# Performance work log

Hardware: AMD Instinct MI355X
Metric: run time of the kernel (lower is better)

The kernel has to match this reference:

```python
import jax, jax.numpy as jnp
import numpy as np

DIM = 4096
N_HEADS = 32
HEAD_DIM = 128
N_KV = 8
REP = N_HEADS // N_KV  # 4
B = 8       # number of packed sequences (block-diagonal blocks)
S = 1024    # tokens per sequence
T = B * S   # seqlen_sum = 8192


def setup_inputs() -> dict:
    key = jax.random.key(0)
    ks = jax.random.split(key, 6)
    x = jax.random.normal(ks[0], (T, DIM), dtype=jnp.float32)
    # RoPE freqs: positions restart at 0 for each packed sequence
    pos = jnp.tile(jnp.arange(S, dtype=jnp.float32), B)            # [T]
    inv_freq = 1.0 / (10000.0 ** (jnp.arange(0, HEAD_DIM, 2, dtype=jnp.float32) / HEAD_DIM))  # [HEAD_DIM//2]
    freqs = pos[:, None] * inv_freq[None, :]                       # [T, HEAD_DIM//2]
    cos = jnp.cos(freqs)
    sin = jnp.sin(freqs)
    s = 0.02
    wq = jax.random.normal(ks[1], (DIM, N_HEADS * HEAD_DIM), dtype=jnp.float32) * s
    wk = jax.random.normal(ks[2], (DIM, N_KV * HEAD_DIM), dtype=jnp.float32) * s
    wv = jax.random.normal(ks[3], (DIM, N_KV * HEAD_DIM), dtype=jnp.float32) * s
    wo = jax.random.normal(ks[4], (N_HEADS * HEAD_DIM, DIM), dtype=jnp.float32) * s
    return {"x": x, "cos": cos, "sin": sin, "wq": wq, "wk": wk, "wv": wv, "wo": wo}


def _rope(t, cos, sin):
    # t: [T, H, D]; cos/sin: [T, D//2]; complex rotation on (even, odd) pairs
    th, hd = t.shape[1], t.shape[2]
    tp = t.reshape(t.shape[0], th, hd // 2, 2)
    te, to = tp[..., 0], tp[..., 1]
    c = cos[:, None, :]
    s = sin[:, None, :]
    oe = te * c - to * s
    oo = te * s + to * c
    return jnp.stack([oe, oo], axis=-1).reshape(t.shape)


def reference(x, cos, sin, wq, wk, wv, wo):
    scale = HEAD_DIM ** -0.5
    q = (x @ wq).reshape(T, N_HEADS, HEAD_DIM)
    k = (x @ wk).reshape(T, N_KV, HEAD_DIM)
    v = (x @ wv).reshape(T, N_KV, HEAD_DIM)
    q = _rope(q, cos, sin)
    k = _rope(k, cos, sin)
    # Block-diagonal mask with equal blocks == batched attention over B sequences.
    # GQA: q head index h = kv*REP + r (matches repeat_interleave on kv dim),
    # so group q heads as [N_KV, REP] instead of materializing repeated K/V.
    q = q.reshape(B, S, N_KV, REP, HEAD_DIM)
    k = k.reshape(B, S, N_KV, HEAD_DIM)
    v = v.reshape(B, S, N_KV, HEAD_DIM)
    scores = jnp.einsum('bqkrd,bskd->bkrqs', q, k) * scale   # [B, N_KV, REP, S, S]
    attn = jax.nn.softmax(scores, axis=-1)
    out = jnp.einsum('bkrqs,bskd->bqkrd', attn, v)           # [B, S, N_KV, REP, D]
    out = out.reshape(T, N_HEADS * HEAD_DIM)
    return out @ wo
```

## Files before the change

### kernel.cpp

```cpp
#include <hip/hip_runtime.h>
#include <math.h>

typedef unsigned short ushort_t;
typedef __attribute__((ext_vector_type(8))) short short8;
typedef __attribute__((ext_vector_type(4))) float f32x4;

#define MFMA16(a, b, c) __builtin_amdgcn_mfma_f32_16x16x32_bf16(a, b, c, 0, 0, 0)

__device__ __forceinline__ ushort_t f2bf(float f) {
    union { float f; unsigned u; } v;
    v.f = f;
    unsigned r = v.u + 0x7FFF + ((v.u >> 16) & 1);
    return (ushort_t)(r >> 16);
}

__device__ __forceinline__ void gload_lds16(const ushort_t* g, ushort_t* l) {
    __builtin_amdgcn_global_load_lds(
        (const __attribute__((address_space(1))) void*)g,
        (__attribute__((address_space(3))) void*)l, 16, 0, 0);
}

__global__ __launch_bounds__(256) void cast_f32_bf16(const float* __restrict__ src,
                                                     ushort_t* __restrict__ dst, int n8) {
    int i = blockIdx.x * 256 + threadIdx.x;
    if (i >= n8) return;
    const float4* s = (const float4*)src;
    float4 a = s[2 * i], b = s[2 * i + 1];
    union { ushort_t u[8]; uint4 v; } o;
    o.u[0] = f2bf(a.x); o.u[1] = f2bf(a.y); o.u[2] = f2bf(a.z); o.u[3] = f2bf(a.w);
    o.u[4] = f2bf(b.x); o.u[5] = f2bf(b.y); o.u[6] = f2bf(b.z); o.u[7] = f2bf(b.w);
    ((uint4*)dst)[i] = o.v;
}

__global__ __launch_bounds__(256) void transpose_cast(const float* __restrict__ src,
                                                      int D, int N,
                                                      ushort_t* __restrict__ dst, int dstStride) {
    __shared__ float t[32][33];
    int n0 = blockIdx.x * 32, d0 = blockIdx.y * 32;
    int tx = threadIdx.x & 31, ty = threadIdx.x >> 5;
#pragma unroll
    for (int i = 0; i < 4; i++)
        t[ty + 8 * i][tx] = src[(size_t)(d0 + ty + 8 * i) * N + n0 + tx];
    __syncthreads();
#pragma unroll
    for (int i = 0; i < 4; i++) {
        int n = ty + 8 * i;
        dst[(size_t)(n0 + n) * dstStride + d0 + tx] = f2bf(t[tx][n]);
    }
}

__global__ __launch_bounds__(256) void transpose_v(const ushort_t* __restrict__ qkv,
                                                   ushort_t* __restrict__ vt) {
    __shared__ ushort_t t[32][33];
    int bk = blockIdx.z; int b = bk >> 3, kvh = bk & 7;
    int s0 = blockIdx.x * 32, d0 = blockIdx.y * 32;
    int tx = threadIdx.x & 31, ty = threadIdx.x >> 5;
#pragma unroll
    for (int i = 0; i < 4; i++)
        t[ty + 8 * i][tx] = qkv[(size_t)(b * 1024 + s0 + ty + 8 * i) * 6144 + 5120 + kvh * 128 + d0 + tx];
    __syncthreads();
#pragma unroll
    for (int i = 0; i < 4; i++)
        vt[((size_t)(b * 8 + kvh) * 128 + d0 + ty + 8 * i) * 1024 + s0 + tx] = t[tx][ty + 8 * i];
}

template <int EPI>
__global__ __launch_bounds__(512, 2) void gemm8x(
    const ushort_t* __restrict__ A, const ushort_t* __restrict__ Bt,
    ushort_t* __restrict__ obf, float* __restrict__ of32,
    int M, int N, int K,
    const float* __restrict__ cosT, const float* __restrict__ sinT) {
    extern __shared__ __align__(16) ushort_t lds[];
    const int tid = threadIdx.x;
    const int lane = tid & 63, wv = tid >> 6;
    const int wr = wv >> 2, wc = wv & 3;
    const int lr = lane & 15, g = lane >> 4;

    const int gx = gridDim.x;
    const int nwg = gx * gridDim.y;
    const int bid = blockIdx.y * gx + blockIdx.x;
    const int swz = (bid & 7) * (nwg >> 3) + (bid >> 3);
    const int brow = (swz / gx) * 256, bcol = (swz % gx) * 256;

    const int st_r = tid >> 3, st_p = tid & 7;
    const int cA = (st_p ^ (st_r & 7)) * 8;
    const size_t aS0 = (size_t)(brow + st_r) * K + cA;
    const size_t bS0 = (size_t)(bcol + st_r) * K + cA;
    const int dstT = st_r * 64 + st_p * 8;

    const int sl0 = (g ^ (lr & 7)) * 8;
    const int sl1 = ((4 + g) ^ (lr & 7)) * 8;
    const int aRow = (wr * 128 + lr) * 64;
    const int bRow = (wc * 64 + lr) * 64;

    f32x4 acc[8][4];
#pragma unroll
    for (int m = 0; m < 8; m++)
#pragma unroll
        for (int n = 0; n < 4; n++) acc[m][n] = (f32x4){0.f, 0.f, 0.f, 0.f};

#define STG_A(kn, roff)                                                          \
    gload_lds16(A + aS0 + (size_t)(roff) * K + (size_t)(kn) * 64,                \
                lds + ((kn) & 1) * 16384 + (roff) * 64 + dstT)
#define STG_B(kn, roff)                                                          \
    gload_lds16(Bt + bS0 + (size_t)(roff) * K + (size_t)(kn) * 64,               \
                lds + 32768 + ((kn) & 1) * 16384 + (roff) * 64 + dstT)

    STG_B(0, 0);  STG_B(0, 64);
    STG_B(0, 128); STG_B(0, 192);
    STG_A(0, 0);  STG_A(0, 128);
    STG_A(0, 64); STG_A(0, 192);

    const int NKT = K >> 6;
    for (int kt = 0; kt < NKT; ++kt) {
        const int buf = (kt & 1) * 16384;
        const bool stg = kt < NKT - 1;
        const int kn = kt + 1;

        asm volatile("s_waitcnt vmcnt(2)" ::: "memory");
        __builtin_amdgcn_sched_barrier(0);
        __builtin_amdgcn_s_barrier();
        __builtin_amdgcn_sched_barrier(0);
        if (stg) { STG_B(kn, 0); STG_B(kn, 64); STG_B(kn, 128); STG_B(kn, 192); }
        short8 bfr[2][4], af[2][4];
#pragma unroll
        for (int n = 0; n < 4; ++n) {
            bfr[0][n] = *(const short8*)(lds + 32768 + buf + bRow + n * 1024 + sl0);
            bfr[1][n] = *(const short8*)(lds + 32768 + buf + bRow + n * 1024 + sl1);
        }
#pragma unroll
        for (int m = 0; m < 4; ++m) {
            af[0][m] = *(const short8*)(lds + buf + aRow + m * 1024 + sl0);
            af[1][m] = *(const short8*)(lds + buf + aRow + m * 1024 + sl1);
        }
        __builtin_amdgcn_s_setprio(1);
#pragma unroll
        for (int ks = 0; ks < 2; ++ks)
#pragma unroll
            for (int m = 0; m < 4; ++m)
#pragma unroll
                for (int n = 0; n < 4; ++n)
                    acc[m][n] = MFMA16(af[ks][m], bfr[ks][n], acc[m][n]);
        __builtin_amdgcn_s_setprio(0);

        if (stg) asm volatile("s_waitcnt vmcnt(4)" ::: "memory");
        else     asm volatile("s_waitcnt vmcnt(0)" ::: "memory");
        __builtin_amdgcn_sched_barrier(0);
        __builtin_amdgcn_s_barrier();
        __builtin_amdgcn_sched_barrier(0);
        if (stg) { STG_A(kn, 0); STG_A(kn, 128); STG_A(kn, 64); STG_A(kn, 192); }
#pragma unroll
        for (int m = 0; m < 4; ++m) {
            af[0][m] = *(const short8*)(lds + buf + aRow + 4096 + m * 1024 + sl0);
            af[1][m] = *(const short8*)(lds + buf + aRow + 4096 + m * 1024 + sl1);
        }
        __builtin_amdgcn_s_setprio(1);
#pragma unroll
        for (int ks = 0; ks < 2; ++ks)
#pragma unroll
            for (int m = 0; m < 4; ++m)
#pragma unroll
                for (int n = 0; n < 4; ++n)
                    acc[m + 4][n] = MFMA16(af[ks][m], bfr[ks][n], acc[m + 4][n]);
        __builtin_amdgcn_s_setprio(0);
    }
#undef STG_A
#undef STG_B

#pragma unroll
    for (int m = 0; m < 8; ++m) {
#pragma unroll
        for (int n = 0; n < 4; ++n) {
#pragma unroll
            for (int reg = 0; reg < 4; ++reg) {
                int r = brow + wr * 128 + m * 16 + g * 4 + reg;
                int c = bcol + wc * 64 + n * 16 + lr;
                float val = acc[m][n][reg];
                if (EPI == 1) {
                    float other = __shfl_xor(val, 1, 64);
                    if (c < 5120) {
                        int pos = r & 1023;
                        int pair = (c & 127) >> 1;
                        float cz = cosT[pos * 64 + pair];
                        float sz = sinT[pos * 64 + pair];
                        val = val * cz + other * ((c & 1) ? sz : -sz);
                        if (c < 4096) val *= 0.12752551286084110f;
                    }
                    obf[(size_t)r * N + c] = f2bf(val);
                } else {
                    of32[(size_t)r * N + c] = val;
                }
            }
        }
    }
}

__global__ __launch_bounds__(512, 2) void attn_fwd2(const ushort_t* __restrict__ qkv,
                                                    const ushort_t* __restrict__ vt,
                                                    ushort_t* __restrict__ aout) {
    extern __shared__ __align__(16) ushort_t lds[];
    const int tid = threadIdx.x, lane = tid & 63, w = tid >> 6;
    const int lr = lane & 15, g = lane >> 4;
    const int hr = w & 3, qc = w >> 2;
    const int qt = blockIdx.x, kvh = blockIdx.y, b = blockIdx.z;
    const int h = kvh * 4 + hr;
    const size_t qRow0 = (size_t)b * 1024 + qt * 64 + qc * 32;
    const size_t kBase = (size_t)b * 1024 * 6144 + 4096 + kvh * 128;
    const size_t vBase = (size_t)(b * 8 + kvh) * 128 * 1024;
    ushort_t* Pw = lds + 32768 + w * 2304;

    short8 qf[2][4];
#pragma unroll
    for (int qg = 0; qg < 2; ++qg)
#pragma unroll
        for (int kd = 0; kd < 4; ++kd)
            qf[qg][kd] = *(const short8*)&qkv[(qRow0 + qg * 16 + lr) * 6144 + h * 128 + kd * 32 + g * 8];

    f32x4 o[2][8];
#pragma unroll
    for (int qg = 0; qg < 2; ++qg)
#pragma unroll
        for (int nd = 0; nd < 8; ++nd) o[qg][nd] = (f32x4){0.f, 0.f, 0.f, 0.f};
    f32x4 lsum[2];
    lsum[0] = (f32x4){0.f, 0.f, 0.f, 0.f};
    lsum[1] = (f32x4){0.f, 0.f, 0.f, 0.f};

#define STAGE_KV(kt)                                                                   \
    {                                                                                  \
        const int buf_ = (kt) & 1;                                                     \
        {                                                                              \
            const int r0_ = tid >> 4, p_ = tid & 15;                                   \
            gload_lds16(qkv + kBase + (size_t)((kt) * 64 + r0_) * 6144 + ((p_ ^ (r0_ & 7)) * 8), \
                        lds + buf_ * 8192 + r0_ * 128 + p_ * 8);                       \
            const int r1_ = r0_ + 32;                                                  \
            gload_lds16(qkv + kBase + (size_t)((kt) * 64 + r1_) * 6144 + ((p_ ^ (r1_ & 7)) * 8), \
                        lds + buf_ * 8192 + r1_ * 128 + p_ * 8);                       \
        }                                                                              \
        {                                                                              \
            const int d0_ = tid >> 3, p_ = tid & 7;                                    \
            gload_lds16(vt + vBase + (size_t)d0_ * 1024 + (kt) * 64 + ((p_ ^ (d0_ & 7)) * 8), \
                        lds + 16384 + buf_ * 8192 + d0_ * 64 + p_ * 8);                \
            const int d1_ = d0_ + 64;                                                  \
            gload_lds16(vt + vBase + (size_t)d1_ * 1024 + (kt) * 64 + ((p_ ^ (d1_ & 7)) * 8), \
                        lds + 16384 + buf_ * 8192 + d1_ * 64 + p_ * 8);                \
        }                                                                              \
    }

    STAGE_KV(0);

    for (int kt = 0; kt < 16; ++kt) {
        const int buf = kt & 1;
        if (kt < 15) {
            STAGE_KV(kt + 1);
            asm volatile("s_waitcnt vmcnt(4)" ::: "memory");
        } else {
            asm volatile("s_waitcnt vmcnt(0)" ::: "memory");
        }
        __builtin_amdgcn_s_barrier();

        f32x4 sc[2][4];
#pragma unroll
        for (int qg = 0; qg < 2; ++qg)
#pragma unroll
            for (int ns = 0; ns < 4; ++ns) sc[qg][ns] = (f32x4){0.f, 0.f, 0.f, 0.f};
        __builtin_amdgcn_s_setprio(1);
#pragma unroll
        for (int ns = 0; ns < 4; ++ns) {
            const int key = ns * 16 + lr;
#pragma unroll
            for (int kd = 0; kd < 4; ++kd) {
                const short8 kf = *(const short8*)(lds + buf * 8192 + key * 128 +
                                                   (((kd * 4 + g) ^ (lr & 7)) * 8));
                sc[0][ns] = MFMA16(qf[0][kd], kf, sc[0][ns]);
                sc[1][ns] = MFMA16(qf[1][kd], kf, sc[1][ns]);
            }
        }
        __builtin_amdgcn_s_setprio(0);

#pragma unroll
        for (int qg = 0; qg < 2; ++qg) {
#pragma unroll
            for (int ns = 0; ns < 4; ++ns) {
#pragma unroll
                for (int j = 0; j < 4; ++j) {
                    float p = exp2f(sc[qg][ns][j]);
                    sc[qg][ns][j] = p;
                    lsum[qg][j] += p;
                }
            }
        }
#pragma unroll
        for (int qg = 0; qg < 2; ++qg)
#pragma unroll
            for (int ns = 0; ns < 4; ++ns)
#pragma unroll
                for (int j = 0; j < 4; ++j)
                    Pw[(qg * 16 + g * 4 + j) * 72 + ns * 16 + lr] = f2bf(sc[qg][ns][j]);

        __builtin_amdgcn_s_setprio(1);
#pragma unroll
        for (int ks = 0; ks < 2; ++ks) {
            short8 pa[2];
            pa[0] = *(const short8*)(Pw + (0 + lr) * 72 + ks * 32 + g * 8);
            pa[1] = *(const short8*)(Pw + (16 + lr) * 72 + ks * 32 + g * 8);
#pragma unroll
            for (int nd = 0; nd < 8; ++nd) {
                const int d = nd * 16 + lr;
                const short8 vf = *(const short8*)(lds + 16384 + buf * 8192 + d * 64 +
                                                   (((ks * 4 + g) ^ (d & 7)) * 8));
                o[0][nd] = MFMA16(pa[0], vf, o[0][nd]);
                o[1][nd] = MFMA16(pa[1], vf, o[1][nd]);
            }
        }
        __builtin_amdgcn_s_setprio(0);
        __builtin_amdgcn_s_barrier();
    }
#undef STAGE_KV

#pragma unroll
    for (int qg = 0; qg < 2; ++qg) {
#pragma unroll
        for (int j = 0; j < 4; ++j) {
            float s = lsum[qg][j];
            s += __shfl_xor(s, 1, 64);
            s += __shfl_xor(s, 2, 64);
            s += __shfl_xor(s, 4, 64);
            s += __shfl_xor(s, 8, 64);
            const float inv = 1.0f / s;
            const size_t r = qRow0 + qg * 16 + g * 4 + j;
#pragma unroll
            for (int nd = 0; nd < 8; ++nd)
                aout[r * 4096 + h * 128 + nd * 16 + lr] = f2bf(o[qg][nd][j] * inv);
        }
    }
}

extern "C" void kernel_launch(void* const* d_in, const int* in_sizes, int n_in,
                              void* d_out, int out_size, void* d_ws, size_t ws_size,
                              hipStream_t stream) {
    const float* x    = (const float*)d_in[0];
    const float* cosT = (const float*)d_in[1];
    const float* sinT = (const float*)d_in[2];
    const float* wq   = (const float*)d_in[3];
    const float* wk   = (const float*)d_in[4];
    const float* wv   = (const float*)d_in[5];
    const float* wo   = (const float*)d_in[6];
    float* out = (float*)d_out;

    char* ws = (char*)d_ws;
    ushort_t* xb   = (ushort_t*)(ws);
    ushort_t* wT   = (ushort_t*)(ws + 67108864);
    ushort_t* woT  = (ushort_t*)(ws + 117440512);
    ushort_t* qkv  = (ushort_t*)(ws + 150994944);
    ushort_t* vtb  = (ushort_t*)(ws + 67108864);
    ushort_t* attn = (ushort_t*)(ws);

    hipFuncSetAttribute((const void*)gemm8x<1>, hipFuncAttributeMaxDynamicSharedMemorySize, 131072);
    hipFuncSetAttribute((const void*)gemm8x<2>, hipFuncAttributeMaxDynamicSharedMemorySize, 131072);
    hipFuncSetAttribute((const void*)attn_fwd2, hipFuncAttributeMaxDynamicSharedMemorySize, 102400);

    cast_f32_bf16<<<16384, 256, 0, stream>>>(x, xb, 8192 * 4096 / 8);
    transpose_cast<<<dim3(128, 128), 256, 0, stream>>>(wq, 4096, 4096, wT, 4096);
    transpose_cast<<<dim3(32, 128), 256, 0, stream>>>(wk, 4096, 1024, wT + (size_t)4096 * 4096, 4096);
    transpose_cast<<<dim3(32, 128), 256, 0, stream>>>(wv, 4096, 1024, wT + (size_t)5120 * 4096, 4096);
    transpose_cast<<<dim3(128, 128), 256, 0, stream>>>(wo, 4096, 4096, woT, 4096);

    gemm8x<1><<<dim3(24, 32), 512, 131072, stream>>>(xb, wT, qkv, nullptr, 8192, 6144, 4096, cosT, sinT);
    transpose_v<<<dim3(32, 4, 64), 256, 0, stream>>>(qkv, vtb);
    attn_fwd2<<<dim3(16, 8, 8), 512, 102400, stream>>>(qkv, vtb, attn);
    gemm8x<2><<<dim3(16, 32), 512, 131072, stream>>>(attn, woT, nullptr, out, 8192, 4096, 4096, nullptr, nullptr);
}
```

Measured before the change: 958.8 us.

## Restructure GEMM main loop with triple-buffered A and finer-grained staging

```diff
diff --git a/kernel.cpp b/kernel.cpp
--- a/kernel.cpp
+++ b/kernel.cpp
@@ -32,20 +32,25 @@
     ((uint4*)dst)[i] = o.v;
 }
 
-__global__ __launch_bounds__(256) void transpose_cast(const float* __restrict__ src,
-                                                      int D, int N,
-                                                      ushort_t* __restrict__ dst, int dstStride) {
-    __shared__ float t[32][33];
-    int n0 = blockIdx.x * 32, d0 = blockIdx.y * 32;
-    int tx = threadIdx.x & 31, ty = threadIdx.x >> 5;
-#pragma unroll
-    for (int i = 0; i < 4; i++)
-        t[ty + 8 * i][tx] = src[(size_t)(d0 + ty + 8 * i) * N + n0 + tx];
+__global__ __launch_bounds__(256) void transpose_cast64(const float* __restrict__ src,
+                                                        int D, int N,
+                                                        ushort_t* __restrict__ dst, int dstStride) {
+    __shared__ float t[64][33];
+    int n0 = blockIdx.x * 32, d0 = blockIdx.y * 64;
+    {
+        int tx = threadIdx.x & 31, ty = threadIdx.x >> 5;
+#pragma unroll
+        for (int i = 0; i < 8; i++)
+            t[ty + 8 * i][tx] = src[(size_t)(d0 + ty + 8 * i) * N + n0 + tx];
+    }
     __syncthreads();
-#pragma unroll
-    for (int i = 0; i < 4; i++) {
-        int n = ty + 8 * i;
-        dst[(size_t)(n0 + n) * dstStride + d0 + tx] = f2bf(t[tx][n]);
+    {
+        int tx = threadIdx.x & 63, ty = threadIdx.x >> 6;
+#pragma unroll
+        for (int i = 0; i < 8; i++) {
+            int n = ty + 4 * i;
+            dst[(size_t)(n0 + n) * dstStride + d0 + tx] = f2bf(t[tx][n]);
+        }
     }
 }
 
@@ -65,7 +70,7 @@
 }
 
 template <int EPI>
-__global__ __launch_bounds__(512, 2) void gemm8x(
+__global__ __launch_bounds__(512, 2) void gemm17(
     const ushort_t* __restrict__ A, const ushort_t* __restrict__ Bt,
     ushort_t* __restrict__ obf, float* __restrict__ of32,
     int M, int N, int K,
@@ -84,14 +89,22 @@
 
     const int st_r = tid >> 3, st_p = tid & 7;
     const int cA = (st_p ^ (st_r & 7)) * 8;
-    const size_t aS0 = (size_t)(brow + st_r) * K + cA;
-    const size_t bS0 = (size_t)(bcol + st_r) * K + cA;
     const int dstT = st_r * 64 + st_p * 8;
+
+    const ushort_t* sAq[4];
+    const ushort_t* sBq[4];
+#pragma unroll
+    for (int q = 0; q < 4; ++q) {
+        sAq[q] = A + (size_t)(brow + q * 64 + st_r) * K + cA;
+        sBq[q] = Bt + (size_t)(bcol + q * 64 + st_r) * K + cA;
+    }
 
     const int sl0 = (g ^ (lr & 7)) * 8;
     const int sl1 = ((4 + g) ^ (lr & 7)) * 8;
-    const int aRow = (wr * 128 + lr) * 64;
-    const int bRow = (wc * 64 + lr) * 64;
+    const ushort_t* pA0 = lds + (wr * 128 + lr) * 64 + sl0;
+    const ushort_t* pA1 = lds + (wr * 128 + lr) * 64 + sl1;
+    const ushort_t* pB0 = lds + 49152 + (wc * 64 + lr) * 64 + sl0;
+    const ushort_t* pB1 = lds + 49152 + (wc * 64 + lr) * 64 + sl1;
 
     f32x4 acc[8][4];
 #pragma unroll
@@ -99,71 +112,93 @@
 #pragma unroll
         for (int n = 0; n < 4; n++) acc[m][n] = (f32x4){0.f, 0.f, 0.f, 0.f};
 
-#define STG_A(kn, roff)                                                          \
-    gload_lds16(A + aS0 + (size_t)(roff) * K + (size_t)(kn) * 64,                \
-                lds + ((kn) & 1) * 16384 + (roff) * 64 + dstT)
-#define STG_B(kn, roff)                                                          \
-    gload_lds16(Bt + bS0 + (size_t)(roff) * K + (size_t)(kn) * 64,               \
-                lds + 32768 + ((kn) & 1) * 16384 + (roff) * 64 + dstT)
-
-    STG_B(0, 0);  STG_B(0, 64);
-    STG_B(0, 128); STG_B(0, 192);
-    STG_A(0, 0);  STG_A(0, 128);
-    STG_A(0, 64); STG_A(0, 192);
-
-    const int NKT = K >> 6;
-    for (int kt = 0; kt < NKT; ++kt) {
-        const int buf = (kt & 1) * 16384;
-        const bool stg = kt < NKT - 1;
-        const int kn = kt + 1;
-
-        asm volatile("s_waitcnt vmcnt(2)" ::: "memory");
-        __builtin_amdgcn_sched_barrier(0);
-        __builtin_amdgcn_s_barrier();
-        __builtin_amdgcn_sched_barrier(0);
-        if (stg) { STG_B(kn, 0); STG_B(kn, 64); STG_B(kn, 128); STG_B(kn, 192); }
-        short8 bfr[2][4], af[2][4];
-#pragma unroll
-        for (int n = 0; n < 4; ++n) {
-            bfr[0][n] = *(const short8*)(lds + 32768 + buf + bRow + n * 1024 + sl0);
-            bfr[1][n] = *(const short8*)(lds + 32768 + buf + bRow + n * 1024 + sl1);
-        }
-#pragma unroll
-        for (int m = 0; m < 4; ++m) {
-            af[0][m] = *(const short8*)(lds + buf + aRow + m * 1024 + sl0);
-            af[1][m] = *(const short8*)(lds + buf + aRow + m * 1024 + sl1);
-        }
-        __builtin_amdgcn_s_setprio(1);
-#pragma unroll
-        for (int ks = 0; ks < 2; ++ks)
-#pragma unroll
-            for (int m = 0; m < 4; ++m)
-#pragma unroll
-                for (int n = 0; n < 4; ++n)
-                    acc[m][n] = MFMA16(af[ks][m], bfr[ks][n], acc[m][n]);
-        __builtin_amdgcn_s_setprio(0);
-
-        if (stg) asm volatile("s_waitcnt vmcnt(4)" ::: "memory");
-        else     asm volatile("s_waitcnt vmcnt(0)" ::: "memory");
-        __builtin_amdgcn_sched_barrier(0);
-        __builtin_amdgcn_s_barrier();
-        __builtin_amdgcn_sched_barrier(0);
-        if (stg) { STG_A(kn, 0); STG_A(kn, 128); STG_A(kn, 64); STG_A(kn, 192); }
-#pragma unroll
-        for (int m = 0; m < 4; ++m) {
-            af[0][m] = *(const short8*)(lds + buf + aRow + 4096 + m * 1024 + sl0);
-            af[1][m] = *(const short8*)(lds + buf + aRow + 4096 + m * 1024 + sl1);
-        }
-        __builtin_amdgcn_s_setprio(1);
-#pragma unroll
-        for (int ks = 0; ks < 2; ++ks)
-#pragma unroll
-            for (int m = 0; m < 4; ++m)
-#pragma unroll
-                for (int n = 0; n < 4; ++n)
-                    acc[m + 4][n] = MFMA16(af[ks][m], bfr[ks][n], acc[m + 4][n]);
-        __builtin_amdgcn_s_setprio(0);
-    }
+#define STG_A(kn, q, SLOT) \
+    gload_lds16(sAq[q] + (size_t)(kn) * 64, lds + (SLOT) * 16384 + (q) * 4096 + dstT)
+#define STG_B(kn, q, SLOT) \
+    gload_lds16(sBq[q] + (size_t)(kn) * 64, lds + 49152 + (SLOT) * 16384 + (q) * 4096 + dstT)
+
+    STG_B(0, 0, 0); STG_B(0, 1, 0); STG_B(0, 2, 0); STG_B(0, 3, 0);
+    STG_A(0, 0, 0); STG_A(0, 1, 0); STG_A(0, 2, 0); STG_A(0, 3, 0);
+    STG_A(1, 0, 1); STG_A(1, 1, 1); STG_A(1, 2, 1); STG_A(1, 3, 1);
+
+#define TILE(SA, SB, kt, LAST)                                                       \
+    {                                                                                \
+        short8 bfr[4], af[4];                                                        \
+                        \
+        if (LAST) asm volatile("s_waitcnt vmcnt(0)" ::: "memory");                   \
+        else      asm volatile("s_waitcnt vmcnt(4)" ::: "memory");                   \
+        __builtin_amdgcn_s_barrier();                                                \
+        __builtin_amdgcn_sched_barrier(0);                                           \
+        _Pragma("unroll")                                                            \
+        for (int n = 0; n < 4; ++n)                                                  \
+            bfr[n] = *(const short8*)(pB0 + (SB) * 16384 + n * 1024);                \
+        _Pragma("unroll")                                                            \
+        for (int m = 0; m < 4; ++m)                                                  \
+            af[m] = *(const short8*)(pA0 + (SA) * 16384 + m * 1024);                 \
+        if ((kt) + 1 < 64) { STG_B((kt) + 1, 0, (SB) ^ 1); STG_B((kt) + 1, 1, (SB) ^ 1); } \
+        __builtin_amdgcn_s_setprio(1);                                               \
+        _Pragma("unroll")                                                            \
+        for (int m = 0; m < 4; ++m)                                                  \
+            _Pragma("unroll")                                                        \
+            for (int n = 0; n < 4; ++n) acc[m][n] = MFMA16(af[m], bfr[n], acc[m][n]); \
+        __builtin_amdgcn_s_setprio(0);                                               \
+          \
+        __builtin_amdgcn_s_barrier();                                                \
+        __builtin_amdgcn_sched_barrier(0);                                           \
+        _Pragma("unroll")                                                            \
+        for (int m = 0; m < 4; ++m)                                                  \
+            af[m] = *(const short8*)(pA0 + (SA) * 16384 + 4096 + m * 1024);          \
+        if ((kt) + 1 < 64) { STG_B((kt) + 1, 2, (SB) ^ 1); STG_B((kt) + 1, 3, (SB) ^ 1); } \
+        __builtin_amdgcn_s_setprio(1);                                               \
+        _Pragma("unroll")                                                            \
+        for (int m = 0; m < 4; ++m)                                                  \
+            _Pragma("unroll")                                                        \
+            for (int n = 0; n < 4; ++n) acc[m + 4][n] = MFMA16(af[m], bfr[n], acc[m + 4][n]); \
+        __builtin_amdgcn_s_setprio(0);                                               \
+                                                       \
+        __builtin_amdgcn_s_barrier();                                                \
+        __builtin_amdgcn_sched_barrier(0);                                           \
+        _Pragma("unroll")                                                            \
+        for (int n = 0; n < 4; ++n)                                                  \
+            bfr[n] = *(const short8*)(pB1 + (SB) * 16384 + n * 1024);                \
+        _Pragma("unroll")                                                            \
+        for (int m = 0; m < 4; ++m)                                                  \
+            af[m] = *(const short8*)(pA1 + (SA) * 16384 + m * 1024);                 \
+        if ((kt) + 2 < 64) { STG_A((kt) + 2, 0, ((SA) + 2) % 3); STG_A((kt) + 2, 1, ((SA) + 2) % 3); } \
+        __builtin_amdgcn_s_setprio(1);                                               \
+        _Pragma("unroll")                                                            \
+        for (int m = 0; m < 4; ++m)                                                  \
+            _Pragma("unroll")                                                        \
+            for (int n = 0; n < 4; ++n) acc[m][n] = MFMA16(af[m], bfr[n], acc[m][n]); \
+        __builtin_amdgcn_s_setprio(0);                                               \
+                                                       \
+        __builtin_amdgcn_s_barrier();                                                \
+        __builtin_amdgcn_sched_barrier(0);                                           \
+        _Pragma("unroll")                                                            \
+        for (int m = 0; m < 4; ++m)                                                  \
+            af[m] = *(const short8*)(pA1 + (SA) * 16384 + 4096 + m * 1024);          \
+        if ((kt) + 2 < 64) { STG_A((kt) + 2, 2, ((SA) + 2) % 3); STG_A((kt) + 2, 3, ((SA) + 2) % 3); } \
+        __builtin_amdgcn_s_setprio(1);                                               \
+        _Pragma("unroll")                                                            \
+        for (int m = 0; m < 4; ++m)                                                  \
+            _Pragma("unroll")                                                        \
+            for (int n = 0; n < 4; ++n) acc[m + 4][n] = MFMA16(af[m], bfr[n], acc[m + 4][n]); \
+        __builtin_amdgcn_s_setprio(0);                                               \
+    }
+
+    for (int kt0 = 0; kt0 < 60; kt0 += 6) {
+        TILE(0, 0, kt0 + 0, false);
+        TILE(1, 1, kt0 + 1, false);
+        TILE(2, 0, kt0 + 2, false);
+        TILE(0, 1, kt0 + 3, false);
+        TILE(1, 0, kt0 + 4, false);
+        TILE(2, 1, kt0 + 5, false);
+    }
+    TILE(0, 0, 60, false);
+    TILE(1, 1, 61, false);
+    TILE(2, 0, 62, false);
+    TILE(0, 1, 63, true);
+#undef TILE
 #undef STG_A
 #undef STG_B
 
@@ -355,18 +390,18 @@
     ushort_t* vtb  = (ushort_t*)(ws + 67108864);
     ushort_t* attn = (ushort_t*)(ws);
 
-    hipFuncSetAttribute((const void*)gemm8x<1>, hipFuncAttributeMaxDynamicSharedMemorySize, 131072);
-    hipFuncSetAttribute((const void*)gemm8x<2>, hipFuncAttributeMaxDynamicSharedMemorySize, 131072);
+    hipFuncSetAttribute((const void*)gemm17<1>, hipFuncAttributeMaxDynamicSharedMemorySize, 163840);
+    hipFuncSetAttribute((const void*)gemm17<2>, hipFuncAttributeMaxDynamicSharedMemorySize, 163840);
     hipFuncSetAttribute((const void*)attn_fwd2, hipFuncAttributeMaxDynamicSharedMemorySize, 102400);
 
     cast_f32_bf16<<<16384, 256, 0, stream>>>(x, xb, 8192 * 4096 / 8);
-    transpose_cast<<<dim3(128, 128), 256, 0, stream>>>(wq, 4096, 4096, wT, 4096);
-    transpose_cast<<<dim3(32, 128), 256, 0, stream>>>(wk, 4096, 1024, wT + (size_t)4096 * 4096, 4096);
-    transpose_cast<<<dim3(32, 128), 256, 0, stream>>>(wv, 4096, 1024, wT + (size_t)5120 * 4096, 4096);
-    transpose_cast<<<dim3(128, 128), 256, 0, stream>>>(wo, 4096, 4096, woT, 4096);
-
-    gemm8x<1><<<dim3(24, 32), 512, 131072, stream>>>(xb, wT, qkv, nullptr, 8192, 6144, 4096, cosT, sinT);
+    transpose_cast64<<<dim3(128, 64), 256, 0, stream>>>(wq, 4096, 4096, wT, 4096);
+    transpose_cast64<<<dim3(32, 64), 256, 0, stream>>>(wk, 4096, 1024, wT + (size_t)4096 * 4096, 4096);
+    transpose_cast64<<<dim3(32, 64), 256, 0, stream>>>(wv, 4096, 1024, wT + (size_t)5120 * 4096, 4096);
+    transpose_cast64<<<dim3(128, 64), 256, 0, stream>>>(wo, 4096, 4096, woT, 4096);
+
+    gemm17<1><<<dim3(24, 32), 512, 163840, stream>>>(xb, wT, qkv, nullptr, 8192, 6144, 4096, cosT, sinT);
     transpose_v<<<dim3(32, 4, 64), 256, 0, stream>>>(qkv, vtb);
     attn_fwd2<<<dim3(16, 8, 8), 512, 102400, stream>>>(qkv, vtb, attn);
-    gemm8x<2><<<dim3(16, 32), 512, 131072, stream>>>(attn, woT, nullptr, out, 8192, 4096, 4096, nullptr, nullptr);
-}
+    gemm17<2><<<dim3(16, 32), 512, 163840, stream>>>(attn, woT, nullptr, out, 8192, 4096, 4096, nullptr, nullptr);
+}
```

Result: faster. 911.1 us, median of 3 (-5.0%).
